# Kernel optimization log

Hardware: AMD Instinct MI355X
Metric: run time of the kernel (lower is better)

## Reference

```python
import jax, jax.numpy as jnp
import numpy as np

B, R, D = 16, 360, 64  # batch, roi_num, input_dim


def setup_inputs() -> dict:
    key = jax.random.key(0)
    ks = jax.random.split(key, 5)
    scale_out = 1.0 / np.sqrt(2 * D)
    scale_cat = 1.0 / np.sqrt(D)
    return {
        "x": jax.random.normal(ks[0], (B, R, D), dtype=jnp.float32),
        # torch Linear stores [out,in]; we store transposed [in,out] for x @ W
        "W_out": jax.random.uniform(ks[1], (2 * D, D), jnp.float32, -scale_out, scale_out),
        "b_out": jax.random.uniform(ks[2], (D,), jnp.float32, -scale_out, scale_out),
        "W_cat": jax.random.uniform(ks[3], (D, 1), jnp.float32, -scale_cat, scale_cat),
        "b_cat": jax.random.uniform(ks[4], (1,), jnp.float32, -scale_cat, scale_cat),
    }


def reference(x, W_out, b_out, W_cat, b_cat):
    b, r, _ = x.shape
    # rel_rec/rel_send are one-hot over np.where(ones([R,R])) -> row-major
    # rows = repeat(arange(R), R) (receivers), cols = tile(arange(R), R) (senders).
    rec_idx = jnp.repeat(jnp.arange(r), r)   # [R*R]
    send_idx = jnp.tile(jnp.arange(r), r)    # [R*R]
    receivers = x[:, rec_idx]                # [B, R*R, D] gather, not dense GEMM
    senders = x[:, send_idx]                 # [B, R*R, D]
    h = jnp.concatenate([senders, receivers], axis=2)        # [B, R*R, 2D]
    h = jax.nn.relu(jnp.einsum('bef,fd->bed', h, W_out) + b_out)  # [B, R*R, D]
    out = jax.nn.relu(jnp.einsum('bed,do->beo', h, W_cat) + b_cat)  # [B, R*R, 1]
    return out.reshape(b, r, r, -1)
```

## Files before the change

kernel.cpp:

```cpp
#include <hip/hip_runtime.h>

#define BATCH 16
#define RR    360
#define DD    64
#define RPB   16
#define TI    8

typedef _Float16 h2 __attribute__((ext_vector_type(2)));

__global__ __launch_bounds__(256) void precompute_st(
    const float* __restrict__ x, const float* __restrict__ Wout,
    const float* __restrict__ bout, const float* __restrict__ wcat,
    _Float16* __restrict__ s_h, _Float16* __restrict__ t_h,
    _Float16* __restrict__ w_h)
{
    __shared__ float WTs[DD * 68];
    __shared__ float WTt[DD * 68];
    __shared__ float xl[RPB * DD];

    const int tid  = threadIdx.x;
    const int row0 = blockIdx.x * RPB;

    #pragma unroll
    for (int it = 0; it < 32; ++it) {
        const int e = tid + it * 256;
        const int f = e >> 6, d = e & 63;
        const float v = Wout[e];
        if (f < DD) WTs[d * 68 + f] = v;
        else        WTt[d * 68 + (f - DD)] = v;
    }
    {
        const float4* x4 = (const float4*)(x + (size_t)row0 * DD);
        ((float4*)xl)[tid] = x4[tid];
    }
    if (blockIdx.x == 0 && tid < DD) w_h[tid] = (_Float16)wcat[tid];

    __syncthreads();

    const int d   = tid & 63;
    const int sub = tid >> 6;
    const float bv = bout[d];

    float ws[DD], wt[DD];
    #pragma unroll
    for (int k = 0; k < DD / 4; ++k) {
        const float4 a = *(const float4*)&WTs[d * 68 + 4 * k];
        ws[4*k] = a.x; ws[4*k+1] = a.y; ws[4*k+2] = a.z; ws[4*k+3] = a.w;
        const float4 c = *(const float4*)&WTt[d * 68 + 4 * k];
        wt[4*k] = c.x; wt[4*k+1] = c.y; wt[4*k+2] = c.z; wt[4*k+3] = c.w;
    }

    #pragma unroll
    for (int q = 0; q < 4; ++q) {
        const int r = sub * 4 + q;
        float sa = 0.f, ta = bv;
        #pragma unroll
        for (int k = 0; k < DD / 4; ++k) {
            const float4 xv = *(const float4*)&xl[r * DD + 4 * k];
            sa = fmaf(xv.x, ws[4*k  ], sa);  ta = fmaf(xv.x, wt[4*k  ], ta);
            sa = fmaf(xv.y, ws[4*k+1], sa);  ta = fmaf(xv.y, wt[4*k+1], ta);
            sa = fmaf(xv.z, ws[4*k+2], sa);  ta = fmaf(xv.z, wt[4*k+2], ta);
            sa = fmaf(xv.w, ws[4*k+3], sa);  ta = fmaf(xv.w, wt[4*k+3], ta);
        }
        s_h[(size_t)(row0 + r) * DD + d] = (_Float16)sa;
        t_h[(size_t)(row0 + r) * DD + d] = (_Float16)ta;
    }
}

__global__ __launch_bounds__(384) void pairwise_out(
    const h2* __restrict__ s_h, const h2* __restrict__ t_h,
    const h2* __restrict__ w_h, const float* __restrict__ bcat,
    float* __restrict__ out)
{
    const int tid = threadIdx.x;
    const int b   = blockIdx.y;
    const int i0  = blockIdx.x * TI;
    const float bc = bcat[0];

    h2 wl[DD / 2];
    #pragma unroll
    for (int k = 0; k < DD / 2; ++k) wl[k] = w_h[k];

    const int j = tid;
    if (j >= RR) return;

    h2 sr[DD / 2];
    const h2* srow = s_h + ((size_t)b * RR + j) * (DD / 2);
    #pragma unroll
    for (int k = 0; k < DD / 2; ++k) sr[k] = srow[k];

    h2 zero; zero.x = (_Float16)0; zero.y = (_Float16)0;

    float* orow = out + ((size_t)b * RR * RR + (size_t)i0 * RR + j);
    const h2* tbase = t_h + ((size_t)b * RR + i0) * (DD / 2);

    #pragma unroll
    for (int ii = 0; ii < TI; ++ii) {
        const h2* trow = tbase + ii * (DD / 2);
        float acc = bc;
        #pragma unroll
        for (int k = 0; k < DD / 2; ++k) {
            h2 p = sr[k] + trow[k];
            p = __builtin_elementwise_max(p, zero);
#if __has_builtin(__builtin_amdgcn_fdot2)
            acc = __builtin_amdgcn_fdot2(p, wl[k], acc, false);
#else
            acc = fmaf((float)p.x, (float)wl[k].x, acc);
            acc = fmaf((float)p.y, (float)wl[k].y, acc);
#endif
        }
        acc = acc > 0.f ? acc : 0.f;
        orow[(size_t)ii * RR] = acc;
    }
}

extern "C" void kernel_launch(void* const* d_in, const int* in_sizes, int n_in,
                              void* d_out, int out_size, void* d_ws, size_t ws_size,
                              hipStream_t stream) {
    const float* x    = (const float*)d_in[0];
    const float* Wout = (const float*)d_in[1];
    const float* bout = (const float*)d_in[2];
    const float* Wcat = (const float*)d_in[3];
    const float* bcat = (const float*)d_in[4];
    float* out = (float*)d_out;

    _Float16* s_h = (_Float16*)d_ws;
    _Float16* t_h = s_h + (size_t)BATCH * RR * DD;
    _Float16* w_h = t_h + (size_t)BATCH * RR * DD;

    precompute_st<<<dim3(BATCH * RR / RPB), dim3(256), 0, stream>>>(
        x, Wout, bout, Wcat, s_h, t_h, w_h);
    pairwise_out<<<dim3(RR / TI, BATCH), dim3(384), 0, stream>>>(
        (const h2*)s_h, (const h2*)t_h, (const h2*)w_h, bcat, out);
}
```

Before: 78.88 us.

## Fuse projection precompute into pairwise kernel with LDS-resident sender tiles

Merges the two kernels into one. Each block recomputes the full sender projection for its batch into swizzled shared memory, plus the receiver projection for its 24-row tile. This removes the second launch and the global fp16 workspace round trip. In exchange, every block redundantly recomputes all 360 sender rows, and the larger tile leaves fewer blocks (240) with heavier shared memory use. The inner dot product is also split into two accumulators for ILP.

Result: slower. 109.6 us (+39.0%).

```diff
diff --git a/kernel.cpp b/kernel.cpp
--- a/kernel.cpp
+++ b/kernel.cpp
@@ -3,43 +3,41 @@
 #define BATCH 16
 #define RR    360
 #define DD    64
-#define RPB   16
-#define TI    8
+#define TI    24
+#define NBLK  (RR / TI)
+#define CH    60
+#define NCH   (RR / CH)
+#define NT    384
 
 typedef _Float16 h2 __attribute__((ext_vector_type(2)));
+typedef _Float16 h8 __attribute__((ext_vector_type(8)));
 
-__global__ __launch_bounds__(256) void precompute_st(
+__global__ __launch_bounds__(NT) void fused_pairwise(
     const float* __restrict__ x, const float* __restrict__ Wout,
     const float* __restrict__ bout, const float* __restrict__ wcat,
-    _Float16* __restrict__ s_h, _Float16* __restrict__ t_h,
-    _Float16* __restrict__ w_h)
+    const float* __restrict__ bcat, float* __restrict__ out)
 {
-    __shared__ float WTs[DD * 68];
-    __shared__ float WTt[DD * 68];
-    __shared__ float xl[RPB * DD];
+    __shared__ __align__(16) _Float16 s_tile[RR * DD];
+    __shared__ __align__(16) _Float16 t_tile[TI * DD];
+    __shared__ __align__(16) float    xl[CH * DD];
 
-    const int tid  = threadIdx.x;
-    const int row0 = blockIdx.x * RPB;
-
-    #pragma unroll
-    for (int it = 0; it < 32; ++it) {
-        const int e = tid + it * 256;
-        const int f = e >> 6, d = e & 63;
-        const float v = Wout[e];
-        if (f < DD) WTs[d * 68 + f] = v;
-        else        WTt[d * 68 + (f - DD)] = v;
-    }
-    {
-        const float4* x4 = (const float4*)(x + (size_t)row0 * DD);
-        ((float4*)xl)[tid] = x4[tid];
-    }
-    if (blockIdx.x == 0 && tid < DD) w_h[tid] = (_Float16)wcat[tid];
-
-    __syncthreads();
-
+    const int tid = threadIdx.x;
+    const int b   = blockIdx.y;
+    const int i0  = blockIdx.x * TI;
     const int d   = tid & 63;
     const int sub = tid >> 6;
+
+    float* WTs = (float*)s_tile;
+    float* WTt = WTs + DD * 68;
+    for (int e = tid; e < 2 * DD * DD; e += NT) {
+        const int f = e >> 6, dd = e & 63;
+        const float v = Wout[e];
+        if (f < DD) WTs[dd * 68 + f] = v;
+        else        WTt[dd * 68 + (f - DD)] = v;
+    }
+    ((float4*)xl)[tid] = ((const float4*)(x + ((size_t)b * RR + i0) * DD))[tid];
     const float bv = bout[d];
+    __syncthreads();
 
     float ws[DD], wt[DD];
     #pragma unroll
@@ -51,72 +49,98 @@
     }
 
     #pragma unroll
-    for (int q = 0; q < 4; ++q) {
-        const int r = sub * 4 + q;
-        float sa = 0.f, ta = bv;
+    for (int qq = 0; qq < TI / 6; ++qq) {
+        const int q = sub * (TI / 6) + qq;
+        const float4* xr = (const float4*)&xl[q * DD];
+        float a0 = bv, a1 = 0.f;
         #pragma unroll
         for (int k = 0; k < DD / 4; ++k) {
-            const float4 xv = *(const float4*)&xl[r * DD + 4 * k];
-            sa = fmaf(xv.x, ws[4*k  ], sa);  ta = fmaf(xv.x, wt[4*k  ], ta);
-            sa = fmaf(xv.y, ws[4*k+1], sa);  ta = fmaf(xv.y, wt[4*k+1], ta);
-            sa = fmaf(xv.z, ws[4*k+2], sa);  ta = fmaf(xv.z, wt[4*k+2], ta);
-            sa = fmaf(xv.w, ws[4*k+3], sa);  ta = fmaf(xv.w, wt[4*k+3], ta);
+            const float4 xv = xr[k];
+            a0 = fmaf(xv.x, wt[4*k  ], a0);
+            a1 = fmaf(xv.y, wt[4*k+1], a1);
+            a0 = fmaf(xv.z, wt[4*k+2], a0);
+            a1 = fmaf(xv.w, wt[4*k+3], a1);
         }
-        s_h[(size_t)(row0 + r) * DD + d] = (_Float16)sa;
-        t_h[(size_t)(row0 + r) * DD + d] = (_Float16)ta;
+        t_tile[q * DD + d] = (_Float16)(a0 + a1);
     }
-}
+    __syncthreads();
 
-__global__ __launch_bounds__(384) void pairwise_out(
-    const h2* __restrict__ s_h, const h2* __restrict__ t_h,
-    const h2* __restrict__ w_h, const float* __restrict__ bcat,
-    float* __restrict__ out)
-{
-    const int tid = threadIdx.x;
-    const int b   = blockIdx.y;
-    const int i0  = blockIdx.x * TI;
-    const float bc = bcat[0];
+    for (int c = 0; c < NCH; ++c) {
+        const float4* xsrc = (const float4*)(x + ((size_t)b * RR + c * CH) * DD);
+        for (int e = tid; e < CH * DD / 4; e += NT) ((float4*)xl)[e] = xsrc[e];
+        __syncthreads();
+        #pragma unroll 2
+        for (int m = 0; m < CH / 6; ++m) {
+            const int rl = sub + 6 * m;
+            const int r  = c * CH + rl;
+            const float4* xr = (const float4*)&xl[rl * DD];
+            float a0 = 0.f, a1 = 0.f;
+            #pragma unroll
+            for (int k = 0; k < DD / 4; ++k) {
+                const float4 xv = xr[k];
+                a0 = fmaf(xv.x, ws[4*k  ], a0);
+                a1 = fmaf(xv.y, ws[4*k+1], a1);
+                a0 = fmaf(xv.z, ws[4*k+2], a0);
+                a1 = fmaf(xv.w, ws[4*k+3], a1);
+            }
+            const int pc = (d >> 3) ^ (r & 7);
+            s_tile[r * DD + pc * 8 + (d & 7)] = (_Float16)(a0 + a1);
+        }
+        __syncthreads();
+    }
 
     h2 wl[DD / 2];
     #pragma unroll
-    for (int k = 0; k < DD / 2; ++k) wl[k] = w_h[k];
+    for (int k = 0; k < DD / 2; ++k) {
+        h2 w; w.x = (_Float16)wcat[2*k]; w.y = (_Float16)wcat[2*k+1];
+        wl[k] = w;
+    }
+    const float bc = bcat[0];
 
     const int j = tid;
     if (j >= RR) return;
 
     h2 sr[DD / 2];
-    const h2* srow = s_h + ((size_t)b * RR + j) * (DD / 2);
     #pragma unroll
-    for (int k = 0; k < DD / 2; ++k) sr[k] = srow[k];
+    for (int k = 0; k < DD / 8; ++k) {
+        const int pc = k ^ (j & 7);
+        union { h8 v; h2 p[4]; } u;
+        u.v = *(const h8*)&s_tile[j * DD + pc * 8];
+        sr[4*k+0] = u.p[0]; sr[4*k+1] = u.p[1]; sr[4*k+2] = u.p[2]; sr[4*k+3] = u.p[3];
+    }
 
     h2 zero; zero.x = (_Float16)0; zero.y = (_Float16)0;
+    float* orow = out + ((size_t)b * RR * RR + (size_t)i0 * RR + j);
 
-    float* orow = out + ((size_t)b * RR * RR + (size_t)i0 * RR + j);
-    const h2* tbase = t_h + ((size_t)b * RR + i0) * (DD / 2);
-
-    #pragma unroll
+    #pragma unroll 4
     for (int ii = 0; ii < TI; ++ii) {
-        const h2* trow = tbase + ii * (DD / 2);
-        float acc = bc;
+        const h2* trow = (const h2*)&t_tile[ii * DD];
+        float a0 = bc, a1 = 0.f;
         #pragma unroll
-        for (int k = 0; k < DD / 2; ++k) {
-            h2 p = sr[k] + trow[k];
-            p = __builtin_elementwise_max(p, zero);
+        for (int k = 0; k < DD / 2; k += 2) {
+            h2 p0 = sr[k]   + trow[k];
+            h2 p1 = sr[k+1] + trow[k+1];
+            p0 = __builtin_elementwise_max(p0, zero);
+            p1 = __builtin_elementwise_max(p1, zero);
 #if __has_builtin(__builtin_amdgcn_fdot2)
-            acc = __builtin_amdgcn_fdot2(p, wl[k], acc, false);
+            a0 = __builtin_amdgcn_fdot2(p0, wl[k],   a0, false);
+            a1 = __builtin_amdgcn_fdot2(p1, wl[k+1], a1, false);
 #else
-            acc = fmaf((float)p.x, (float)wl[k].x, acc);
-            acc = fmaf((float)p.y, (float)wl[k].y, acc);
+            a0 = fmaf((float)p0.x, (float)wl[k].x,   a0);
+            a0 = fmaf((float)p0.y, (float)wl[k].y,   a0);
+            a1 = fmaf((float)p1.x, (float)wl[k+1].x, a1);
+            a1 = fmaf((float)p1.y, (float)wl[k+1].y, a1);
 #endif
         }
-        acc = acc > 0.f ? acc : 0.f;
-        orow[(size_t)ii * RR] = acc;
+        const float acc = a0 + a1;
+        orow[(size_t)ii * RR] = acc > 0.f ? acc : 0.f;
     }
 }
 
 extern "C" void kernel_launch(void* const* d_in, const int* in_sizes, int n_in,
                               void* d_out, int out_size, void* d_ws, size_t ws_size,
                               hipStream_t stream) {
+    (void)d_ws; (void)ws_size;
     const float* x    = (const float*)d_in[0];
     const float* Wout = (const float*)d_in[1];
     const float* bout = (const float*)d_in[2];
@@ -124,12 +148,6 @@
     const float* bcat = (const float*)d_in[4];
     float* out = (float*)d_out;
 
-    _Float16* s_h = (_Float16*)d_ws;
-    _Float16* t_h = s_h + (size_t)BATCH * RR * DD;
-    _Float16* w_h = t_h + (size_t)BATCH * RR * DD;
-
-    precompute_st<<<dim3(BATCH * RR / RPB), dim3(256), 0, stream>>>(
-        x, Wout, bout, Wcat, s_h, t_h, w_h);
-    pairwise_out<<<dim3(RR / TI, BATCH), dim3(384), 0, stream>>>(
-        (const h2*)s_h, (const h2*)t_h, (const h2*)w_h, bcat, out);
+    fused_pairwise<<<dim3(NBLK, BATCH), dim3(NT), 0, stream>>>(
+        x, Wout, bout, Wcat, bcat, out);
 }
```
